# Kernel optimization log

Measured on AMD Instinct MI355X. Metric: run time of the kernel, lower is better.

The kernel has to match this reference:

```python
import jax, jax.numpy as jnp
from jax import lax
import numpy as np

NMS_THRESH = 0.5
SCORE_THRESH = 0.05
MAX_DET = 300
B, N, C, P = 8, 20000, 80, 51


def _iou_one_to_many(box, boxes):
    # box: (4,) in (x1,y1,x2,y2); boxes: (N,4). Same IoU math as tf.image.non_max_suppression.
    ix1 = jnp.maximum(box[0], boxes[:, 0])
    iy1 = jnp.maximum(box[1], boxes[:, 1])
    ix2 = jnp.minimum(box[2], boxes[:, 2])
    iy2 = jnp.minimum(box[3], boxes[:, 3])
    inter = jnp.maximum(ix2 - ix1, 0.0) * jnp.maximum(iy2 - iy1, 0.0)
    area_b = (box[2] - box[0]) * (box[3] - box[1])
    area_n = (boxes[:, 2] - boxes[:, 0]) * (boxes[:, 3] - boxes[:, 1])
    union = area_b + area_n - inter
    return jnp.where(union > 0.0, inter / union, 0.0)


def _greedy_nms(boxes, scores):
    """Fixed-length greedy NMS. scores already has -inf at entries below score threshold.
    Returns (idx, keep): idx (MAX_DET,) int32 selected box indices, keep (MAX_DET,) bool validity."""
    bx = lax.stop_gradient(boxes)           # NMS indices are non-differentiable
    s0 = lax.stop_gradient(scores)

    def step(s, _):
        i = jnp.argmax(s)
        ok = s[i] > -jnp.inf
        ious = _iou_one_to_many(bx[i], bx)
        s = jnp.where(ious > NMS_THRESH, -jnp.inf, s)
        s = s.at[i].set(-jnp.inf)
        return s, (i.astype(jnp.int32), ok)

    _, (idx, keep) = lax.scan(step, s0, None, length=MAX_DET)
    return idx, keep


def _filter_one(boxes, classification, relationship):
    # boxes (N,4), classification (N,C), relationship (N,P)
    n_cls = classification.shape[1]
    masked = jnp.where(classification > SCORE_THRESH, classification, -jnp.inf)  # (N,C)
    per_cls = masked.T                                                            # (C,N)

    # class-specific NMS, vectorized over classes
    idx, keep = jax.vmap(lambda s: _greedy_nms(boxes, s))(per_cls)  # (C,MAX_DET) each

    cand = jnp.take_along_axis(per_cls, idx.astype(jnp.int32), axis=1)  # (C,MAX_DET)
    cand = jnp.where(keep, cand, -jnp.inf)

    flat = cand.reshape(-1)                        # (C*MAX_DET,)
    top_s, top_pos = lax.top_k(flat, MAX_DET)      # global top-k over all classes
    box_idx = idx.reshape(-1)[top_pos]             # (MAX_DET,)
    label = top_pos // MAX_DET                     # class id (flatten order (C,M))
    valid = jnp.isfinite(top_s)

    out_boxes = jnp.where(valid[:, None], boxes[box_idx], -1.0)              # (MAX_DET,4)
    out_scores = jnp.where(valid, top_s, -1.0)                               # (MAX_DET,)
    out_labels = jnp.where(valid, label, -1).astype(jnp.int32)

    pred = relationship[box_idx]                                             # (MAX_DET,P)
    pred_labels = jnp.where(valid, jnp.argmax(pred, axis=1), -1).astype(jnp.int32)
    pred_scores = jnp.where(valid, jnp.max(pred, axis=1), -1.0)
    return out_boxes, out_scores, out_labels, pred_scores, pred_labels


def setup_inputs() -> dict:
    key = jax.random.key(0)
    k1, k2, k3, k4 = jax.random.split(key, 4)
    xy = jax.random.uniform(k1, (B, N, 2), dtype=jnp.float32) * 700.0
    wh = jax.random.uniform(k2, (B, N, 2), dtype=jnp.float32) * 100.0 + 1.0
    boxes = jnp.concatenate([xy, xy + wh], axis=-1)                   # valid (x1,y1,x2,y2)
    classification = jax.random.uniform(k3, (B, N, C), dtype=jnp.float32)
    relationship = jax.random.uniform(k4, (B, N, P), dtype=jnp.float32)
    return {"boxes": boxes, "classification": classification, "relationship": relationship}


def reference(boxes, classification, relationship):
    return jax.vmap(_filter_one)(boxes, classification, relationship)
```

## Files before the change

kernel.cpp:

```cpp
#include <hip/hip_runtime.h>
#include <hip/hip_bf16.h>
#include <math.h>

#define NBATCH 8
#define NBOX   20000
#define NCLS   80
#define NREL   51
#define MAXDET 300
#define NTOT   (NCLS * MAXDET)
#define CAP    512
#define SPECCAP 2560
#define NHB    3328
#define HB0    (0x3F666666u >> 9)
#define TARGETK 480u
#define SCORE_THR 0.05f
#define SPEC_THRF 0.9f
#define WWAVES 8

typedef unsigned long long u64;
typedef unsigned int u32;

__device__ __forceinline__ bool iou_sup(float ax1, float ay1, float ax2, float ay2, float aarea,
                                        float bx1, float by1, float bx2, float by2, float barea) {
  float ix1 = fmaxf(ax1, bx1);
  float iy1 = fmaxf(ay1, by1);
  float ix2 = fminf(ax2, bx2);
  float iy2 = fminf(ay2, by2);
  float dw = fmaxf(__fsub_rn(ix2, ix1), 0.0f);
  float dh = fmaxf(__fsub_rn(iy2, iy1), 0.0f);
  float inter = __fmul_rn(dw, dh);
  float uni = __fsub_rn(__fadd_rn(aarea, barea), inter);
  if (!(uni > 0.0f)) return false;
  return __fdiv_rn(inter, uni) > 0.5f;
}

__device__ __forceinline__ bool iou_gt_half(float ax1, float ay1, float ax2, float ay2,
                                            float bx1, float by1, float bx2, float by2) {
  float aa = __fmul_rn(__fsub_rn(ax2, ax1), __fsub_rn(ay2, ay1));
  float ab = __fmul_rn(__fsub_rn(bx2, bx1), __fsub_rn(by2, by1));
  return iou_sup(ax1, ay1, ax2, ay2, aa, bx1, by1, bx2, by2, ab);
}

__device__ __forceinline__ bool iou_sup_fast(float ax1, float ay1, float ax2, float ay2,
                                             float aarea, float bx1, float by1, float bx2,
                                             float by2, float barea) {
  float ix1 = fmaxf(ax1, bx1);
  float iy1 = fmaxf(ay1, by1);
  float ix2 = fminf(ax2, bx2);
  float iy2 = fminf(ay2, by2);
  float dw = fmaxf(__fsub_rn(ix2, ix1), 0.0f);
  float dh = fmaxf(__fsub_rn(iy2, iy1), 0.0f);
  float inter = __fmul_rn(dw, dh);
  float uni = __fsub_rn(__fadd_rn(aarea, barea), inter);
  return (uni > 0.0f) && (inter > __fmul_rn(0.5f, uni));
}

#define CEXR(x, y, asc) { bool sw_ = (asc) ? ((x) > (y)) : ((x) < (y)); \
                          if (sw_) { u64 t_ = (x); (x) = (y); (y) = t_; } }

__device__ __forceinline__ void bitonic_sort(u64* keys, int SZ, int tid) {
  for (int k = 2; k <= SZ; k <<= 1) {
    for (int j = k >> 1; j >= 4; j >>= 1) {
      for (int v = tid; v < (SZ >> 1); v += 256) {
        int i = ((v & ~(j - 1)) << 1) | (v & (j - 1));
        int p = i | j;
        bool asc = ((i & k) == 0);
        u64 a = keys[i], b = keys[p];
        bool sw = asc ? (a > b) : (a < b);
        if (sw) { keys[i] = b; keys[p] = a; }
      }
      __syncthreads();
    }
    if (tid < (SZ >> 2)) {
      ulonglong2* k2 = (ulonglong2*)keys;
      ulonglong2 lo = k2[tid * 2], hi = k2[tid * 2 + 1];
      u64 a = lo.x, b = lo.y, c = hi.x, d = hi.y;
      int i0 = tid << 2;
      if (k == 2) {
        CEXR(a, b, true); CEXR(c, d, false);
      } else {
        bool asc = ((i0 & k) == 0);
        CEXR(a, c, asc); CEXR(b, d, asc);
        CEXR(a, b, asc); CEXR(c, d, asc);
      }
      lo.x = a; lo.y = b; hi.x = c; hi.y = d;
      k2[tid * 2] = lo; k2[tid * 2 + 1] = hi;
    }
    __syncthreads();
  }
}

template <int NB>
__device__ __forceinline__ void suffix_fast(const u32* hist, u32 cap, u32* wsum4, u32* sout) {
  const int tid = threadIdx.x, lane = tid & 63, w = tid >> 6;
  const int G = NB / 256;
  u32 v = 0;
  const int hb = tid * G;
#pragma unroll
  for (int t = 0; t < G; ++t) v += hist[hb + t];
  u32 s = v;
#pragma unroll
  for (int off = 1; off < 64; off <<= 1) {
    u32 t2 = __shfl_down(s, off);
    if (lane + off < 64) s += t2;
  }
  if (lane == 0) wsum4[w] = s;
  __syncthreads();
  u32 total = wsum4[0] + wsum4[1] + wsum4[2] + wsum4[3];
  u32 after = 0;
#pragma unroll
  for (int ww = 1; ww < 4; ++ww) if (ww > w) after += wsum4[ww];
  u32 inc = s + after;
  u32 exc = inc - v;
  if (tid == 0) {
    sout[3] = total;
    if (total == 0u) { sout[0] = 0u; sout[1] = 0u; sout[2] = 0u; }
  }
  u32 target = total < cap ? total : cap;
  if (total != 0u && inc >= target && exc < target) {
    u32 acc = exc;
    for (int u = hb + G - 1; u >= hb; --u) {
      acc += hist[u];
      if (acc >= target) { sout[0] = (u32)u; sout[1] = acc; sout[2] = acc - hist[u]; break; }
    }
  }
  __syncthreads();
}

__global__ __launch_bounds__(256) void k_tr(const float* __restrict__ cls,
                                            float* __restrict__ colS,
                                            u32* __restrict__ ghist,
                                            u32* __restrict__ gtail) {
  __shared__ float tile[NCLS * 65];
  const int tid = threadIdx.x;
  const int b = blockIdx.y;
  const int n0 = blockIdx.x * 64;
  if (blockIdx.x == 0) {
    for (int i = tid; i < NHB; i += 256) ghist[b * NHB + i] = 0u;
    if (tid == 0) gtail[b] = 0u;
  }
  const int rows = (NBOX - n0) < 64 ? (NBOX - n0) : 64;
  const float4* src4 = (const float4*)(cls + ((size_t)b * NBOX + n0) * NCLS);
  const int nq = rows * (NCLS / 4);
  for (int i = tid; i < nq; i += 256) {
    int rr = i / (NCLS / 4);
    int c4 = i - rr * (NCLS / 4);
    float4 v = src4[i];
    tile[(c4 * 4 + 0) * 65 + rr] = v.x;
    tile[(c4 * 4 + 1) * 65 + rr] = v.y;
    tile[(c4 * 4 + 2) * 65 + rr] = v.z;
    tile[(c4 * 4 + 3) * 65 + rr] = v.w;
  }
  __syncthreads();
  float4* dst4 = (float4*)colS;
  for (int i = tid; i < NCLS * 16; i += 256) {
    int c = i >> 4, nl = i & 15;
    if (nl * 4 < rows) {
      float4 v;
      v.x = tile[c * 65 + nl * 4 + 0];
      v.y = tile[c * 65 + nl * 4 + 1];
      v.z = tile[c * 65 + nl * 4 + 2];
      v.w = tile[c * 65 + nl * 4 + 3];
      dst4[(((size_t)b * NCLS + c) * NBOX + n0) / 4 + nl] = v;
    }
  }
}

__global__ __launch_bounds__(256) void k_zero(u32* __restrict__ ghist,
                                              u32* __restrict__ gtail) {
  const int b = blockIdx.x;
  const int tid = threadIdx.x;
  for (int i = tid; i < NHB; i += 256) ghist[b * NHB + i] = 0u;
  if (tid == 0) gtail[b] = 0u;
}

template <int STRIDE>
__device__ __forceinline__ float4 load4s(const float* col, int q) {
  if (STRIDE == 1) return ((const float4*)col)[q];
  float4 v;
  v.x = col[(size_t)(q * 4 + 0) * STRIDE];
  v.y = col[(size_t)(q * 4 + 1) * STRIDE];
  v.z = col[(size_t)(q * 4 + 2) * STRIDE];
  v.w = col[(size_t)(q * 4 + 3) * STRIDE];
  return v;
}

template <int STRIDE>
__global__ __launch_bounds__(256) void k_sel(const float* __restrict__ scores,
                                             u64* __restrict__ keysBase, size_t kstride,
                                             int* __restrict__ selCnt,
                                             int* __restrict__ totCnt,
                                             int* __restrict__ flags) {
  __shared__ __align__(16) char smem[SPECCAP * 8 + NHB * 4 + CAP * 8];
  u64* side = (u64*)smem;
  u32* hist = (u32*)(smem + SPECCAP * 8);
  u64* keys = (u64*)(smem + SPECCAP * 8 + NHB * 4);
  __shared__ u32 wsum[4], selB[4], twave[4];
  __shared__ u32 s_scnt, s_cnt;

  const int tid = threadIdx.x;
  const int lane = tid & 63;
  const int w = tid >> 6;
  const u64 lmask = (1ull << lane) - 1ull;
  const int bc = blockIdx.x;
  const int b = bc / NCLS, c = bc % NCLS;
  const float* col = (STRIDE == 1) ? (scores + (size_t)bc * NBOX)
                                   : (scores + (size_t)b * NBOX * NCLS + c);

  for (int i = tid; i < NHB; i += 256) hist[i] = 0u;
  if (tid == 0) { s_scnt = 0u; s_cnt = 0u; }
  __syncthreads();

  u32 tailc = 0;
  for (int base = 0; base < NBOX / 4; base += 2048) {
    float4 v[8];
#pragma unroll
    for (int p = 0; p < 8; ++p) {
      int q = base + tid + (p << 8);
      if (q < NBOX / 4) v[p] = load4s<STRIDE>(col, q);
    }
#pragma unroll
    for (int p = 0; p < 8; ++p) {
      int q = base + tid + (p << 8);
      if (q < NBOX / 4) {
        float vv[4] = {v[p].x, v[p].y, v[p].z, v[p].w};
#pragma unroll
        for (int e = 0; e < 4; ++e) {
          float s = vv[e];
          bool spec = s > SPEC_THRF;
          if (s > SCORE_THR && !spec) ++tailc;
          u64 mb = __ballot(spec);
          if (mb) {
            u32 bs;
            if (lane == 0) bs = atomicAdd(&s_scnt, (u32)__popcll(mb));
            bs = __shfl(bs, 0);
            if (spec) {
              u32 bits = __float_as_uint(s);
              u32 pos = bs + (u32)__popcll(mb & lmask);
              if (pos < SPECCAP) side[pos] = ((u64)bits << 32) | (~(u32)(q * 4 + e));
              u32 h = (bits >> 9) - HB0;
              if (h > NHB - 1) h = NHB - 1;
              atomicAdd(&hist[h], 1u);
            }
          }
        }
      }
    }
  }
  u32 tr = tailc;
#pragma unroll
  for (int off = 1; off < 64; off <<= 1) tr += __shfl_down(tr, off);
  if (lane == 0) twave[w] = tr;
  __syncthreads();

  const u32 specCount = s_scnt;
  const u32 tailSum = twave[0] + twave[1] + twave[2] + twave[3];
  const u32 totalAll = specCount + tailSum;

  if (totalAll == 0u) {
    if (tid == 0) { selCnt[bc] = 0; totCnt[bc] = 0; flags[bc] = 0; }
    return;
  }
  const u32 target = totalAll < TARGETK ? totalAll : TARGETK;
  if (specCount < target || specCount > SPECCAP) {
    if (tid == 0) { selCnt[bc] = 0; totCnt[bc] = (int)totalAll; flags[bc] = 1; }
    return;
  }

  suffix_fast<NHB>(hist, target, wsum, selB);
  const u32 F0 = selB[0];
  const u32 selCount = selB[1];
  if (selCount > CAP) {
    if (tid == 0) { selCnt[bc] = 0; totCnt[bc] = (int)totalAll; flags[bc] = 1; }
    return;
  }

  const int iters = (int)((specCount + 255u) >> 8);
  for (int it2 = 0; it2 < iters; ++it2) {
    u32 idx = (u32)it2 * 256u + (u32)tid;
    bool act = idx < specCount;
    u64 key = act ? side[idx] : 0ull;
    u32 bits = (u32)(key >> 32);
    u32 h = (bits >> 9) - HB0;
    if (h > NHB - 1) h = NHB - 1;
    bool sel = act && (h >= F0);
    u64 ms = __ballot(sel);
    if (ms) {
      u32 bs;
      if (lane == 0) bs = atomicAdd(&s_cnt, (u32)__popcll(ms));
      bs = __shfl(bs, 0);
      if (sel) keys[bs + (u32)__popcll(ms & lmask)] = key;
    }
  }
  __syncthreads();
  for (int i = (int)selCount + tid; i < CAP; i += 256) keys[i] = 0ull;
  __syncthreads();

  bitonic_sort(keys, CAP, tid);

  u64* kout = keysBase + (size_t)bc * kstride;
  for (int i = tid; i < CAP; i += 256) kout[i] = keys[i];
  if (tid == 0) { selCnt[bc] = (int)selCount; totCnt[bc] = (int)totalAll; flags[bc] = 0; }
}

__device__ void slow_path(const float* __restrict__ boxes,
                          const float* __restrict__ cls, int bc,
                          float* __restrict__ keptScore, int* __restrict__ keptN,
                          int* __restrict__ keptCount,
                          u32* __restrict__ ghist, u32* __restrict__ gtail,
                          char* smem) {
  u32* sup = (u32*)smem;
  u64* red = (u64*)(smem + 2560);
  float4* sbx = (float4*)(smem + 6656);
  int* s_kept = (int*)(smem + 6672);
  const int tid = threadIdx.x;
  const int b = bc / NCLS, c = bc % NCLS;
  const float* col = cls + (size_t)b * NBOX * NCLS + c;

  for (int i = tid; i < (NBOX + 31) / 32; i += 512) sup[i] = 0u;
  if (tid == 0) *s_kept = 0;
  __syncthreads();
  for (int it = 0; it < MAXDET; ++it) {
    u64 best = 0ull;
    for (int n = tid; n < NBOX; n += 512) {
      if ((sup[n >> 5] >> (n & 31)) & 1u) continue;
      float s = col[(size_t)n * NCLS];
      if (s > SCORE_THR) {
        u64 key = ((u64)__float_as_uint(s) << 32) | (~(u32)n);
        if (key > best) best = key;
      }
    }
    red[tid] = best;
    __syncthreads();
    for (int off = 256; off > 0; off >>= 1) {
      if (tid < off) { u64 o = red[tid + off]; if (o > red[tid]) red[tid] = o; }
      __syncthreads();
    }
    u64 win = red[0];
    if (win == 0ull) break;
    u32 nw = ~((u32)win);
    if (tid == 0) {
      int k = *s_kept;
      keptScore[bc * MAXDET + k] = __uint_as_float((u32)(win >> 32));
      keptN[bc * MAXDET + k] = (int)nw;
      *s_kept = k + 1;
      *sbx = ((const float4*)boxes)[(size_t)b * NBOX + nw];
    }
    __syncthreads();
    float4 bx = *sbx;
    for (int n = tid; n < NBOX; n += 512) {
      float4 cb = ((const float4*)boxes)[(size_t)b * NBOX + n];
      if (iou_gt_half(bx.x, bx.y, bx.z, bx.w, cb.x, cb.y, cb.z, cb.w))
        atomicOr(&sup[n >> 5], 1u << (n & 31));
    }
    if (tid == 0) atomicOr(&sup[nw >> 5], 1u << (nw & 31));
    __syncthreads();
  }
  __syncthreads();
  const int kept = *s_kept;
  for (int r = kept + tid; r < MAXDET; r += 512) {
    keptScore[bc * MAXDET + r] = -INFINITY;
    keptN[bc * MAXDET + r] = 0;
  }
  for (int rr = tid; rr < kept; rr += 512) {
    float s = keptScore[bc * MAXDET + rr];
    if (s > SPEC_THRF) {
      u32 h = (__float_as_uint(s) >> 9) - HB0;
      if (h > NHB - 1) h = NHB - 1;
      atomicAdd(&ghist[b * NHB + h], 1u);
    } else {
      atomicAdd(&gtail[b], 1u);
    }
  }
  if (tid == 0) keptCount[bc] = kept;
}

__global__ __launch_bounds__(512) void k_walk(const float* __restrict__ boxes,
                                              const float* __restrict__ cls,
                                              const u64* __restrict__ keysBase, size_t kstride,
                                              const int* __restrict__ selCnt,
                                              const int* __restrict__ totCnt,
                                              float* __restrict__ keptScore,
                                              int* __restrict__ keptN,
                                              int* __restrict__ keptCount,
                                              const int* __restrict__ flags,
                                              u32* __restrict__ ghist,
                                              u32* __restrict__ gtail) {
  __shared__ __align__(16) char smem[22784];
  u64* keys = (u64*)smem;
  float4* candbox = (float4*)(smem + 4096);
  float* carea = (float*)(smem + 12288);
  float4* keptbox = (float4*)(smem + 14336);
  float* karea = (float*)(smem + 19136);
  int* kn = (int*)(smem + 20336);
  float* ksc = (float*)(smem + 21536);
  __shared__ u64 supW[WWAVES];
  __shared__ u64 mpart[WWAVES][64];
  __shared__ int s_kept;

  const int tid = threadIdx.x;
  const int lane = tid & 63;
  const int w = tid >> 6;
  const u64 lmask = (1ull << lane) - 1ull;
  const int bc = blockIdx.x;
  const int b = bc / NCLS;

  if (flags[bc] != 0) {
    slow_path(boxes, cls, bc, keptScore, keptN, keptCount, ghist, gtail, smem);
    return;
  }
  const u32 selCount = (u32)selCnt[bc];
  const u32 totalAll = (u32)totCnt[bc];

  const u64* kin = keysBase + (size_t)bc * kstride;
  for (int i = tid; i < CAP; i += 512) keys[i] = kin[i];
  if (tid == 0) s_kept = 0;
  __syncthreads();

  for (int i = tid; i < (int)selCount; i += 512) {
    int pos = CAP - 1 - i;
    u32 n = ~((u32)keys[pos]);
    float4 bb = ((const float4*)boxes)[(size_t)b * NBOX + n];
    candbox[pos] = bb;
    carea[pos] = __fmul_rn(__fsub_rn(bb.z, bb.x), __fsub_rn(bb.w, bb.y));
  }
  __syncthreads();

  const u32 ntile = (selCount + 63u) >> 6;
  for (u32 t = 0; t < ntile; ++t) {
    const int kept0 = s_kept;
    if (kept0 >= MAXDET) break;
    const u32 r = t * 64u + (u32)lane;
    const bool valid = r < selCount;
    const int si = valid ? (CAP - 1 - (int)r) : (CAP - 1);
    float4 mybox = candbox[si];
    float marea = carea[si];
    bool sup = false;
    for (int k = w; k < kept0; k += WWAVES) {
      float4 kb = keptbox[k];
      if (iou_sup_fast(kb.x, kb.y, kb.z, kb.w, karea[k],
                       mybox.x, mybox.y, mybox.z, mybox.w, marea))
        sup = true;
    }
    u64 bal = __ballot(sup);
    if (lane == 0) supW[w] = bal;
    u64 mw = 0ull;
    const int ebase = w * 8;
#pragma unroll
    for (int ee = 0; ee < 8; ++ee) {
      const int e = ebase + ee;
      int ei = CAP - 1 - (int)(t * 64u) - e;
      float4 eb = candbox[ei];
      if (e < lane && iou_sup_fast(eb.x, eb.y, eb.z, eb.w, carea[ei],
                                   mybox.x, mybox.y, mybox.z, mybox.w, marea))
        mw |= 1ull << e;
    }
    mpart[w][lane] = mw;
    __syncthreads();
    if (w == 0) {
      u64 prior = 0ull, m = 0ull;
#pragma unroll
      for (int ww = 0; ww < WWAVES; ++ww) {
        prior |= supW[ww];
        m |= mpart[ww][lane];
      }
      u64 remaining = __ballot(valid) & ~prior;
      u64 keptmask = 0ull;
      const int room = MAXDET - kept0;
      while (remaining != 0ull && (int)__popcll(keptmask) < room) {
        int j = __ffsll((long long)remaining) - 1;
        keptmask |= 1ull << j;
        remaining &= ~(1ull << j);
        u64 supj = __ballot(((m >> j) & 1ull) != 0ull);
        remaining &= ~supj;
      }
      if ((keptmask >> lane) & 1ull) {
        int pos = kept0 + (int)__popcll(keptmask & lmask);
        u64 mykey = keys[CAP - 1 - (int)r];
        keptbox[pos] = mybox;
        karea[pos] = marea;
        kn[pos] = (int)(~((u32)mykey));
        ksc[pos] = __uint_as_float((u32)(mykey >> 32));
      }
      if (lane == 0) s_kept = kept0 + (int)__popcll(keptmask);
    }
    __syncthreads();
  }

  const int kept = s_kept;
  const bool exhausted = (kept < MAXDET && selCount < totalAll);
  if (exhausted) {
    __syncthreads();
    slow_path(boxes, cls, bc, keptScore, keptN, keptCount, ghist, gtail, smem);
    return;
  }
  for (int rr = tid; rr < MAXDET; rr += 512) {
    keptScore[bc * MAXDET + rr] = (rr < kept) ? ksc[rr] : -INFINITY;
    keptN[bc * MAXDET + rr] = (rr < kept) ? kn[rr] : 0;
  }
  if (tid == 0) keptCount[bc] = kept;
  for (int rr = tid; rr < kept; rr += 512) {
    float s = ksc[rr];
    if (s > SPEC_THRF) {
      u32 h = (__float_as_uint(s) >> 9) - HB0;
      if (h > NHB - 1) h = NHB - 1;
      atomicAdd(&ghist[b * NHB + h], 1u);
    } else {
      atomicAdd(&gtail[b], 1u);
    }
  }
}

__global__ __launch_bounds__(256) void k_osort(const float* __restrict__ boxes,
                                               const float* __restrict__ rel,
                                               const float* __restrict__ keptScore,
                                               const int* __restrict__ keptN,
                                               const u32* __restrict__ ghist,
                                               const u32* __restrict__ gtail,
                                               float* __restrict__ out) {
  __shared__ u64 keys[1024];
  __shared__ u32 wsum[4], selB[4];
  __shared__ u32 s_cnt;
  const int tid = threadIdx.x;
  const int lane = tid & 63;
  const u64 lmask = (1ull << lane) - 1ull;
  const int b = blockIdx.x;
  const float4* ks4 = (const float4*)(keptScore + (size_t)b * NTOT);

  if (tid == 0) s_cnt = 0u;
  suffix_fast<NHB>(ghist + (size_t)b * NHB, (u32)MAXDET, wsum, selB);
  const u32 specTotal = selB[3];
  const u32 totalAll = specTotal + gtail[b];
  const u32 target = totalAll < (u32)MAXDET ? totalAll : (u32)MAXDET;
  const u32 F0 = selB[0];
  const u32 selSpec = selB[1];
  const bool fast = (totalAll != 0u) && (specTotal >= target) && (selSpec <= (u32)CAP);
  int SZ = CAP;

  if (totalAll != 0u) {
    if (fast) {
      for (int base = 0; base < NTOT / 4; base += 2048) {
        float4 v[8];
#pragma unroll
        for (int p = 0; p < 8; ++p) {
          int q = base + tid + (p << 8);
          if (q < NTOT / 4) v[p] = ks4[q];
        }
#pragma unroll
        for (int p = 0; p < 8; ++p) {
          int q = base + tid + (p << 8);
          if (q < NTOT / 4) {
            float vv[4] = {v[p].x, v[p].y, v[p].z, v[p].w};
#pragma unroll
            for (int e = 0; e < 4; ++e) {
              float s = vv[e];
              bool sel = false;
              u32 bits = 0;
              if (s > SPEC_THRF) {
                bits = __float_as_uint(s);
                u32 h = (bits >> 9) - HB0;
                if (h > NHB - 1) h = NHB - 1;
                sel = (h >= F0);
              }
              u64 ms = __ballot(sel);
              if (ms) {
                u32 bs;
                if (lane == 0) bs = atomicAdd(&s_cnt, (u32)__popcll(ms));
                bs = __shfl(bs, 0);
                if (sel)
                  keys[bs + (u32)__popcll(ms & lmask)] =
                      ((u64)bits << 32) | (~(u32)(q * 4 + e));
              }
            }
          }
        }
      }
      __syncthreads();
      for (int i = (int)selSpec + tid; i < CAP; i += 256) keys[i] = 0ull;
      __syncthreads();
      bitonic_sort(keys, CAP, tid);
      SZ = CAP;
    } else {
      if (tid < 64) {
        const int c0 = lane, c1 = 64 + lane;
        const bool has1 = (c1 < NCLS);
        const float* ls0 = keptScore + ((size_t)b * NCLS + c0) * MAXDET;
        const float* ls1 = keptScore + ((size_t)b * NCLS + (has1 ? c1 : c0)) * MAXDET;
        int h0 = 0, h1 = 0;
        float v0 = ls0[0], w0v = ls0[1];
        float v1 = has1 ? ls1[0] : -INFINITY;
        float w1v = has1 ? ls1[1] : -INFINITY;
        for (int r = 0; r < (int)target; ++r) {
          float bs; int bcl;
          if (has1 && v1 > v0) { bs = v1; bcl = c1; } else { bs = v0; bcl = c0; }
#pragma unroll
          for (int off = 32; off > 0; off >>= 1) {
            float os = __shfl_xor(bs, off);
            int oc = __shfl_xor(bcl, off);
            if (os > bs || (os == bs && oc < bcl)) { bs = os; bcl = oc; }
          }
          if (bcl == c0) {
            keys[1023 - r] = ((u64)__float_as_uint(bs) << 32) | (~(u32)(c0 * MAXDET + h0));
            ++h0; v0 = w0v; w0v = (h0 + 1 < MAXDET) ? ls0[h0 + 1] : -INFINITY;
          } else if (has1 && bcl == c1) {
            keys[1023 - r] = ((u64)__float_as_uint(bs) << 32) | (~(u32)(c1 * MAXDET + h1));
            ++h1; v1 = w1v; w1v = (h1 + 1 < MAXDET) ? ls1[h1 + 1] : -INFINITY;
          }
        }
      }
      __syncthreads();
      SZ = 1024;
    }
  }

  for (int r = tid; r < MAXDET; r += 256) {
    const bool valid = (u32)r < target;
    float s = -1.0f, pm = -1.0f, pl = -1.0f, cl = -1.0f;
    float4 ob; ob.x = ob.y = ob.z = ob.w = -1.0f;
    if (valid) {
      u64 key = keys[SZ - 1 - r];
      u32 fp = ~((u32)key);
      int c = (int)(fp / MAXDET);
      int slot = (int)(fp - (u32)c * MAXDET);
      int n = keptN[((size_t)b * NCLS + c) * MAXDET + slot];
      s = __uint_as_float((u32)(key >> 32));
      cl = (float)c;
      size_t nb = (size_t)b * NBOX + (u32)n;
      ob = ((const float4*)boxes)[nb];
      const float* rp = rel + nb * NREL;
      float vr[NREL];
#pragma unroll
      for (int p = 0; p < NREL; ++p) vr[p] = rp[p];
      float best = vr[0]; int bi = 0;
#pragma unroll
      for (int p = 1; p < NREL; ++p) { if (vr[p] > best) { best = vr[p]; bi = p; } }
      pm = best; pl = (float)bi;
    }
    ((float4*)out)[(size_t)b * MAXDET + r] = ob;
    const int sbase = NBATCH * MAXDET * 4;
    out[sbase + b * MAXDET + r] = s;
    out[sbase + NBATCH * MAXDET + b * MAXDET + r] = cl;
    out[sbase + 2 * NBATCH * MAXDET + b * MAXDET + r] = pm;
    out[sbase + 3 * NBATCH * MAXDET + b * MAXDET + r] = pl;
  }
}

extern "C" void kernel_launch(void* const* d_in, const int* in_sizes, int n_in,
                              void* d_out, int out_size, void* d_ws, size_t ws_size,
                              hipStream_t stream) {
  (void)in_sizes; (void)n_in; (void)out_size;
  const float* boxes = (const float*)d_in[0];
  const float* cls   = (const float*)d_in[1];
  const float* rel   = (const float*)d_in[2];
  float* out = (float*)d_out;
  char* ws = (char*)d_ws;

  const size_t trBytes = (size_t)NBATCH * NCLS * NBOX * 4;
  const size_t NP = NBATCH * NCLS;

  float* colS = (float*)ws;
  size_t off = 0;
  const size_t oKeptScore = off; off += NP * MAXDET * 4;
  const size_t oKeptN     = off; off += NP * MAXDET * 4;
  const size_t oKeptCount = off; off += NP * 4;
  const size_t oFlags     = off; off += NP * 4;
  const size_t oSelCnt    = off; off += NP * 4;
  const size_t oTotCnt    = off; off += NP * 4;
  const size_t oKeysSep   = off; off += NP * CAP * 8;
  const size_t oGhist     = off; off += (size_t)NBATCH * NHB * 4;
  const size_t oGtail     = off; off += NBATCH * 4;
  const size_t kbaseBytes = off;

  const bool useTr = ws_size >= trBytes + kbaseBytes;
  char* kbase = useTr ? (ws + trBytes) : ws;

  float* keptScore = (float*)(kbase + oKeptScore);
  int* keptN = (int*)(kbase + oKeptN);
  int* keptCount = (int*)(kbase + oKeptCount);
  int* flags = (int*)(kbase + oFlags);
  int* selCnt = (int*)(kbase + oSelCnt);
  int* totCnt = (int*)(kbase + oTotCnt);
  u64* keysSep = (u64*)(kbase + oKeysSep);
  u32* ghist = (u32*)(kbase + oGhist);
  u32* gtail = (u32*)(kbase + oGtail);

  u64* keysBase = useTr ? (u64*)colS : keysSep;
  const size_t kstride = useTr ? (size_t)(NBOX / 2) : (size_t)CAP;

  if (useTr) {
    k_tr<<<dim3((NBOX + 63) / 64, NBATCH), 256, 0, stream>>>(cls, colS, ghist, gtail);
    k_sel<1><<<NP, 256, 0, stream>>>(colS, keysBase, kstride, selCnt, totCnt, flags);
  } else {
    k_zero<<<NBATCH, 256, 0, stream>>>(ghist, gtail);
    k_sel<NCLS><<<NP, 256, 0, stream>>>(cls, keysBase, kstride, selCnt, totCnt, flags);
  }
  k_walk<<<NP, 512, 0, stream>>>(boxes, cls, keysBase, kstride, selCnt, totCnt,
                                 keptScore, keptN, keptCount, flags, ghist, gtail);
  k_osort<<<NBATCH, 256, 0, stream>>>(boxes, rel, keptScore, keptN, ghist, gtail, out);
}
```

Before: 140.3 us.

## Replace transpose+per-class select with row-major scatter into per-class buckets

Removes the full transpose of the classification tensor and the per-(batch,class) selection kernel. A new scatter kernel reads the classification rows coalesced, counts scores above threshold per class and appends high-score (>0.9) keys into global per-class buckets through global atomics. The histogram, threshold selection and bitonic sort move into the NMS kernel, which now runs them with 512 threads. This cuts one full read/write pass over the scores, at the cost of heavy global atomic contention on 640 counters and non-deterministic key order before sorting.

```diff
diff --git a/kernel.cpp b/kernel.cpp
--- a/kernel.cpp
+++ b/kernel.cpp
@@ -10,12 +10,14 @@
 #define NTOT   (NCLS * MAXDET)
 #define CAP    512
 #define SPECCAP 2560
-#define NHB    3328
+#define NHB    3584
 #define HB0    (0x3F666666u >> 9)
 #define TARGETK 480u
 #define SCORE_THR 0.05f
 #define SPEC_THRF 0.9f
 #define WWAVES 8
+#define QPB    5120
+#define QTOT   (NBOX * NCLS / 4)
 
 typedef unsigned long long u64;
 typedef unsigned int u32;
@@ -58,10 +60,11 @@
 #define CEXR(x, y, asc) { bool sw_ = (asc) ? ((x) > (y)) : ((x) < (y)); \
                           if (sw_) { u64 t_ = (x); (x) = (y); (y) = t_; } }
 
+template <int THREADS>
 __device__ __forceinline__ void bitonic_sort(u64* keys, int SZ, int tid) {
   for (int k = 2; k <= SZ; k <<= 1) {
     for (int j = k >> 1; j >= 4; j >>= 1) {
-      for (int v = tid; v < (SZ >> 1); v += 256) {
+      for (int v = tid; v < (SZ >> 1); v += THREADS) {
         int i = ((v & ~(j - 1)) << 1) | (v & (j - 1));
         int p = i | j;
         bool asc = ((i & k) == 0);
@@ -90,10 +93,11 @@
   }
 }
 
-template <int NB>
-__device__ __forceinline__ void suffix_fast(const u32* hist, u32 cap, u32* wsum4, u32* sout) {
+template <int NB, int THREADS>
+__device__ __forceinline__ void suffix_fast(const u32* hist, u32 cap, u32* wsum, u32* sout) {
   const int tid = threadIdx.x, lane = tid & 63, w = tid >> 6;
-  const int G = NB / 256;
+  const int NW = THREADS / 64;
+  const int G = NB / THREADS;
   u32 v = 0;
   const int hb = tid * G;
 #pragma unroll
@@ -104,12 +108,14 @@
     u32 t2 = __shfl_down(s, off);
     if (lane + off < 64) s += t2;
   }
-  if (lane == 0) wsum4[w] = s;
-  __syncthreads();
-  u32 total = wsum4[0] + wsum4[1] + wsum4[2] + wsum4[3];
+  if (lane == 0) wsum[w] = s;
+  __syncthreads();
+  u32 total = 0;
+#pragma unroll
+  for (int ww = 0; ww < NW; ++ww) total += wsum[ww];
   u32 after = 0;
 #pragma unroll
-  for (int ww = 1; ww < 4; ++ww) if (ww > w) after += wsum4[ww];
+  for (int ww = 1; ww < NW; ++ww) if (ww > w) after += wsum[ww];
   u32 inc = s + after;
   u32 exc = inc - v;
   if (tid == 0) {
@@ -127,180 +133,69 @@
   __syncthreads();
 }
 
-__global__ __launch_bounds__(256) void k_tr(const float* __restrict__ cls,
-                                            float* __restrict__ colS,
-                                            u32* __restrict__ ghist,
-                                            u32* __restrict__ gtail) {
-  __shared__ float tile[NCLS * 65];
-  const int tid = threadIdx.x;
-  const int b = blockIdx.y;
-  const int n0 = blockIdx.x * 64;
-  if (blockIdx.x == 0) {
-    for (int i = tid; i < NHB; i += 256) ghist[b * NHB + i] = 0u;
-    if (tid == 0) gtail[b] = 0u;
-  }
-  const int rows = (NBOX - n0) < 64 ? (NBOX - n0) : 64;
-  const float4* src4 = (const float4*)(cls + ((size_t)b * NBOX + n0) * NCLS);
-  const int nq = rows * (NCLS / 4);
-  for (int i = tid; i < nq; i += 256) {
-    int rr = i / (NCLS / 4);
-    int c4 = i - rr * (NCLS / 4);
-    float4 v = src4[i];
-    tile[(c4 * 4 + 0) * 65 + rr] = v.x;
-    tile[(c4 * 4 + 1) * 65 + rr] = v.y;
-    tile[(c4 * 4 + 2) * 65 + rr] = v.z;
-    tile[(c4 * 4 + 3) * 65 + rr] = v.w;
-  }
-  __syncthreads();
-  float4* dst4 = (float4*)colS;
-  for (int i = tid; i < NCLS * 16; i += 256) {
-    int c = i >> 4, nl = i & 15;
-    if (nl * 4 < rows) {
-      float4 v;
-      v.x = tile[c * 65 + nl * 4 + 0];
-      v.y = tile[c * 65 + nl * 4 + 1];
-      v.z = tile[c * 65 + nl * 4 + 2];
-      v.w = tile[c * 65 + nl * 4 + 3];
-      dst4[(((size_t)b * NCLS + c) * NBOX + n0) / 4 + nl] = v;
-    }
-  }
-}
-
-__global__ __launch_bounds__(256) void k_zero(u32* __restrict__ ghist,
-                                              u32* __restrict__ gtail) {
+__global__ __launch_bounds__(256) void k_init(u32* __restrict__ ghist,
+                                              u32* __restrict__ gtail,
+                                              u32* __restrict__ bucketCnt,
+                                              u32* __restrict__ totCnt) {
   const int b = blockIdx.x;
   const int tid = threadIdx.x;
   for (int i = tid; i < NHB; i += 256) ghist[b * NHB + i] = 0u;
   if (tid == 0) gtail[b] = 0u;
-}
-
-template <int STRIDE>
-__device__ __forceinline__ float4 load4s(const float* col, int q) {
-  if (STRIDE == 1) return ((const float4*)col)[q];
-  float4 v;
-  v.x = col[(size_t)(q * 4 + 0) * STRIDE];
-  v.y = col[(size_t)(q * 4 + 1) * STRIDE];
-  v.z = col[(size_t)(q * 4 + 2) * STRIDE];
-  v.w = col[(size_t)(q * 4 + 3) * STRIDE];
-  return v;
-}
-
-template <int STRIDE>
-__global__ __launch_bounds__(256) void k_sel(const float* __restrict__ scores,
-                                             u64* __restrict__ keysBase, size_t kstride,
-                                             int* __restrict__ selCnt,
-                                             int* __restrict__ totCnt,
-                                             int* __restrict__ flags) {
-  __shared__ __align__(16) char smem[SPECCAP * 8 + NHB * 4 + CAP * 8];
-  u64* side = (u64*)smem;
-  u32* hist = (u32*)(smem + SPECCAP * 8);
-  u64* keys = (u64*)(smem + SPECCAP * 8 + NHB * 4);
-  __shared__ u32 wsum[4], selB[4], twave[4];
-  __shared__ u32 s_scnt, s_cnt;
-
+  for (int i = tid; i < NCLS; i += 256) {
+    bucketCnt[b * NCLS + i] = 0u;
+    totCnt[b * NCLS + i] = 0u;
+  }
+}
+
+__global__ __launch_bounds__(256) void k_scatter(const float* __restrict__ cls,
+                                                 u64* __restrict__ bucketKeys,
+                                                 u32* __restrict__ bucketCnt,
+                                                 u32* __restrict__ totCnt) {
+  __shared__ u32 cnt80[NCLS];
   const int tid = threadIdx.x;
-  const int lane = tid & 63;
-  const int w = tid >> 6;
-  const u64 lmask = (1ull << lane) - 1ull;
-  const int bc = blockIdx.x;
-  const int b = bc / NCLS, c = bc % NCLS;
-  const float* col = (STRIDE == 1) ? (scores + (size_t)bc * NBOX)
-                                   : (scores + (size_t)b * NBOX * NCLS + c);
-
-  for (int i = tid; i < NHB; i += 256) hist[i] = 0u;
-  if (tid == 0) { s_scnt = 0u; s_cnt = 0u; }
-  __syncthreads();
-
-  u32 tailc = 0;
-  for (int base = 0; base < NBOX / 4; base += 2048) {
+  const int b = blockIdx.y;
+  const int q0 = blockIdx.x * QPB;
+  const int qend = (q0 + QPB < QTOT) ? (q0 + QPB) : QTOT;
+  const float4* src = (const float4*)(cls + (size_t)b * NBOX * NCLS);
+  for (int i = tid; i < NCLS; i += 256) cnt80[i] = 0u;
+  __syncthreads();
+
+  for (int base = q0; base < qend; base += 2048) {
     float4 v[8];
 #pragma unroll
     for (int p = 0; p < 8; ++p) {
       int q = base + tid + (p << 8);
-      if (q < NBOX / 4) v[p] = load4s<STRIDE>(col, q);
+      if (q < qend) v[p] = src[q];
     }
 #pragma unroll
     for (int p = 0; p < 8; ++p) {
       int q = base + tid + (p << 8);
-      if (q < NBOX / 4) {
+      if (q < qend) {
+        int n = q / (NCLS / 4);
+        int cb = (q % (NCLS / 4)) * 4;
         float vv[4] = {v[p].x, v[p].y, v[p].z, v[p].w};
 #pragma unroll
         for (int e = 0; e < 4; ++e) {
           float s = vv[e];
-          bool spec = s > SPEC_THRF;
-          if (s > SCORE_THR && !spec) ++tailc;
-          u64 mb = __ballot(spec);
-          if (mb) {
-            u32 bs;
-            if (lane == 0) bs = atomicAdd(&s_scnt, (u32)__popcll(mb));
-            bs = __shfl(bs, 0);
-            if (spec) {
-              u32 bits = __float_as_uint(s);
-              u32 pos = bs + (u32)__popcll(mb & lmask);
-              if (pos < SPECCAP) side[pos] = ((u64)bits << 32) | (~(u32)(q * 4 + e));
-              u32 h = (bits >> 9) - HB0;
-              if (h > NHB - 1) h = NHB - 1;
-              atomicAdd(&hist[h], 1u);
+          if (s > SCORE_THR) {
+            atomicAdd(&cnt80[cb + e], 1u);
+            if (s > SPEC_THRF) {
+              int bkt = b * NCLS + cb + e;
+              u32 pos = atomicAdd(&bucketCnt[bkt], 1u);
+              if (pos < SPECCAP)
+                bucketKeys[(size_t)bkt * SPECCAP + pos] =
+                    ((u64)__float_as_uint(s) << 32) | (~(u32)n);
             }
           }
         }
       }
     }
   }
-  u32 tr = tailc;
-#pragma unroll
-  for (int off = 1; off < 64; off <<= 1) tr += __shfl_down(tr, off);
-  if (lane == 0) twave[w] = tr;
-  __syncthreads();
-
-  const u32 specCount = s_scnt;
-  const u32 tailSum = twave[0] + twave[1] + twave[2] + twave[3];
-  const u32 totalAll = specCount + tailSum;
-
-  if (totalAll == 0u) {
-    if (tid == 0) { selCnt[bc] = 0; totCnt[bc] = 0; flags[bc] = 0; }
-    return;
-  }
-  const u32 target = totalAll < TARGETK ? totalAll : TARGETK;
-  if (specCount < target || specCount > SPECCAP) {
-    if (tid == 0) { selCnt[bc] = 0; totCnt[bc] = (int)totalAll; flags[bc] = 1; }
-    return;
-  }
-
-  suffix_fast<NHB>(hist, target, wsum, selB);
-  const u32 F0 = selB[0];
-  const u32 selCount = selB[1];
-  if (selCount > CAP) {
-    if (tid == 0) { selCnt[bc] = 0; totCnt[bc] = (int)totalAll; flags[bc] = 1; }
-    return;
-  }
-
-  const int iters = (int)((specCount + 255u) >> 8);
-  for (int it2 = 0; it2 < iters; ++it2) {
-    u32 idx = (u32)it2 * 256u + (u32)tid;
-    bool act = idx < specCount;
-    u64 key = act ? side[idx] : 0ull;
-    u32 bits = (u32)(key >> 32);
-    u32 h = (bits >> 9) - HB0;
-    if (h > NHB - 1) h = NHB - 1;
-    bool sel = act && (h >= F0);
-    u64 ms = __ballot(sel);
-    if (ms) {
-      u32 bs;
-      if (lane == 0) bs = atomicAdd(&s_cnt, (u32)__popcll(ms));
-      bs = __shfl(bs, 0);
-      if (sel) keys[bs + (u32)__popcll(ms & lmask)] = key;
-    }
-  }
-  __syncthreads();
-  for (int i = (int)selCount + tid; i < CAP; i += 256) keys[i] = 0ull;
-  __syncthreads();
-
-  bitonic_sort(keys, CAP, tid);
-
-  u64* kout = keysBase + (size_t)bc * kstride;
-  for (int i = tid; i < CAP; i += 256) kout[i] = keys[i];
-  if (tid == 0) { selCnt[bc] = (int)selCount; totCnt[bc] = (int)totalAll; flags[bc] = 0; }
+  __syncthreads();
+  for (int c = tid; c < NCLS; c += 256) {
+    u32 v = cnt80[c];
+    if (v) atomicAdd(&totCnt[b * NCLS + c], v);
+  }
 }
 
 __device__ void slow_path(const float* __restrict__ boxes,
@@ -375,25 +270,28 @@
   if (tid == 0) keptCount[bc] = kept;
 }
 
-__global__ __launch_bounds__(512) void k_walk(const float* __restrict__ boxes,
-                                              const float* __restrict__ cls,
-                                              const u64* __restrict__ keysBase, size_t kstride,
-                                              const int* __restrict__ selCnt,
-                                              const int* __restrict__ totCnt,
-                                              float* __restrict__ keptScore,
-                                              int* __restrict__ keptN,
-                                              int* __restrict__ keptCount,
-                                              const int* __restrict__ flags,
-                                              u32* __restrict__ ghist,
-                                              u32* __restrict__ gtail) {
-  __shared__ __align__(16) char smem[22784];
-  u64* keys = (u64*)smem;
-  float4* candbox = (float4*)(smem + 4096);
-  float* carea = (float*)(smem + 12288);
-  float4* keptbox = (float4*)(smem + 14336);
-  float* karea = (float*)(smem + 19136);
-  int* kn = (int*)(smem + 20336);
-  float* ksc = (float*)(smem + 21536);
+__global__ __launch_bounds__(512) void k_nms(const float* __restrict__ boxes,
+                                             const float* __restrict__ cls,
+                                             const u64* __restrict__ bucketKeys,
+                                             const u32* __restrict__ bucketCnt,
+                                             const u32* __restrict__ totCnt,
+                                             float* __restrict__ keptScore,
+                                             int* __restrict__ keptN,
+                                             int* __restrict__ keptCount,
+                                             u32* __restrict__ ghist,
+                                             u32* __restrict__ gtail) {
+  __shared__ __align__(16) char smem[38912];
+  u64* side = (u64*)smem;
+  u32* hist = (u32*)(smem + 20480);
+  u64* keys = (u64*)(smem + 34816);
+  float4* candbox = (float4*)smem;
+  float* carea = (float*)(smem + 8192);
+  float4* keptbox = (float4*)(smem + 10240);
+  float* karea = (float*)(smem + 15040);
+  int* kn = (int*)(smem + 16240);
+  float* ksc = (float*)(smem + 17440);
+  __shared__ u32 wsum[WWAVES], selB[4];
+  __shared__ u32 s_cnt;
   __shared__ u64 supW[WWAVES];
   __shared__ u64 mpart[WWAVES][64];
   __shared__ int s_kept;
@@ -405,17 +303,68 @@
   const int bc = blockIdx.x;
   const int b = bc / NCLS;
 
-  if (flags[bc] != 0) {
+  const u32 specRaw = bucketCnt[bc];
+  const u32 totalAll = totCnt[bc];
+
+  if (totalAll == 0u) {
+    for (int r = tid; r < MAXDET; r += 512) {
+      keptScore[bc * MAXDET + r] = -INFINITY;
+      keptN[bc * MAXDET + r] = 0;
+    }
+    if (tid == 0) keptCount[bc] = 0;
+    return;
+  }
+  const u32 target = totalAll < TARGETK ? totalAll : TARGETK;
+  if (specRaw > SPECCAP || specRaw < target) {
     slow_path(boxes, cls, bc, keptScore, keptN, keptCount, ghist, gtail, smem);
     return;
   }
-  const u32 selCount = (u32)selCnt[bc];
-  const u32 totalAll = (u32)totCnt[bc];
-
-  const u64* kin = keysBase + (size_t)bc * kstride;
-  for (int i = tid; i < CAP; i += 512) keys[i] = kin[i];
-  if (tid == 0) s_kept = 0;
-  __syncthreads();
+  const u32 specCount = specRaw;
+
+  const u64* bk = bucketKeys + (size_t)bc * SPECCAP;
+  for (int i = tid; i < (int)specCount; i += 512) side[i] = bk[i];
+  for (int i = tid; i < NHB; i += 512) hist[i] = 0u;
+  if (tid == 0) { s_cnt = 0u; s_kept = 0; }
+  __syncthreads();
+  for (int i = tid; i < (int)specCount; i += 512) {
+    u32 bits = (u32)(side[i] >> 32);
+    u32 h = (bits >> 9) - HB0;
+    if (h > NHB - 1) h = NHB - 1;
+    atomicAdd(&hist[h], 1u);
+  }
+  __syncthreads();
+
+  suffix_fast<NHB, 512>(hist, target, wsum, selB);
+  const u32 F0 = selB[0];
+  const u32 selCount = selB[1];
+  if (selCount > CAP) {
+    __syncthreads();
+    slow_path(boxes, cls, bc, keptScore, keptN, keptCount, ghist, gtail, smem);
+    return;
+  }
+
+  const int iters = (int)((specCount + 511u) >> 9);
+  for (int it2 = 0; it2 < iters; ++it2) {
+    u32 idx = (u32)it2 * 512u + (u32)tid;
+    bool act = idx < specCount;
+    u64 key = act ? side[idx] : 0ull;
+    u32 bits = (u32)(key >> 32);
+    u32 h = (bits >> 9) - HB0;
+    if (h > NHB - 1) h = NHB - 1;
+    bool sel = act && (h >= F0);
+    u64 ms = __ballot(sel);
+    if (ms) {
+      u32 bs;
+      if (lane == 0) bs = atomicAdd(&s_cnt, (u32)__popcll(ms));
+      bs = __shfl(bs, 0);
+      if (sel) keys[bs + (u32)__popcll(ms & lmask)] = key;
+    }
+  }
+  __syncthreads();
+  for (int i = (int)selCount + tid; i < CAP; i += 512) keys[i] = 0ull;
+  __syncthreads();
+
+  bitonic_sort<512>(keys, CAP, tid);
 
   for (int i = tid; i < (int)selCount; i += 512) {
     int pos = CAP - 1 - i;
@@ -528,7 +477,7 @@
   const float4* ks4 = (const float4*)(keptScore + (size_t)b * NTOT);
 
   if (tid == 0) s_cnt = 0u;
-  suffix_fast<NHB>(ghist + (size_t)b * NHB, (u32)MAXDET, wsum, selB);
+  suffix_fast<NHB, 256>(ghist + (size_t)b * NHB, (u32)MAXDET, wsum, selB);
   const u32 specTotal = selB[3];
   const u32 totalAll = specTotal + gtail[b];
   const u32 target = totalAll < (u32)MAXDET ? totalAll : (u32)MAXDET;
@@ -578,7 +527,7 @@
       __syncthreads();
       for (int i = (int)selSpec + tid; i < CAP; i += 256) keys[i] = 0ull;
       __syncthreads();
-      bitonic_sort(keys, CAP, tid);
+      bitonic_sort<256>(keys, CAP, tid);
       SZ = CAP;
     } else {
       if (tid < 64) {
@@ -648,53 +597,40 @@
 extern "C" void kernel_launch(void* const* d_in, const int* in_sizes, int n_in,
                               void* d_out, int out_size, void* d_ws, size_t ws_size,
                               hipStream_t stream) {
-  (void)in_sizes; (void)n_in; (void)out_size;
+  (void)in_sizes; (void)n_in; (void)out_size; (void)ws_size;
   const float* boxes = (const float*)d_in[0];
   const float* cls   = (const float*)d_in[1];
   const float* rel   = (const float*)d_in[2];
   float* out = (float*)d_out;
   char* ws = (char*)d_ws;
 
-  const size_t trBytes = (size_t)NBATCH * NCLS * NBOX * 4;
   const size_t NP = NBATCH * NCLS;
-
-  float* colS = (float*)ws;
   size_t off = 0;
   const size_t oKeptScore = off; off += NP * MAXDET * 4;
   const size_t oKeptN     = off; off += NP * MAXDET * 4;
   const size_t oKeptCount = off; off += NP * 4;
-  const size_t oFlags     = off; off += NP * 4;
-  const size_t oSelCnt    = off; off += NP * 4;
+  const size_t oBucketCnt = off; off += NP * 4;
   const size_t oTotCnt    = off; off += NP * 4;
-  const size_t oKeysSep   = off; off += NP * CAP * 8;
+  const size_t oGtail     = off; off += NBATCH * 4;
+  off = (off + 7) & ~(size_t)7;
   const size_t oGhist     = off; off += (size_t)NBATCH * NHB * 4;
-  const size_t oGtail     = off; off += NBATCH * 4;
-  const size_t kbaseBytes = off;
-
-  const bool useTr = ws_size >= trBytes + kbaseBytes;
-  char* kbase = useTr ? (ws + trBytes) : ws;
-
-  float* keptScore = (float*)(kbase + oKeptScore);
-  int* keptN = (int*)(kbase + oKeptN);
-  int* keptCount = (int*)(kbase + oKeptCount);
-  int* flags = (int*)(kbase + oFlags);
-  int* selCnt = (int*)(kbase + oSelCnt);
-  int* totCnt = (int*)(kbase + oTotCnt);
-  u64* keysSep = (u64*)(kbase + oKeysSep);
-  u32* ghist = (u32*)(kbase + oGhist);
-  u32* gtail = (u32*)(kbase + oGtail);
-
-  u64* keysBase = useTr ? (u64*)colS : keysSep;
-  const size_t kstride = useTr ? (size_t)(NBOX / 2) : (size_t)CAP;
-
-  if (useTr) {
-    k_tr<<<dim3((NBOX + 63) / 64, NBATCH), 256, 0, stream>>>(cls, colS, ghist, gtail);
-    k_sel<1><<<NP, 256, 0, stream>>>(colS, keysBase, kstride, selCnt, totCnt, flags);
-  } else {
-    k_zero<<<NBATCH, 256, 0, stream>>>(ghist, gtail);
-    k_sel<NCLS><<<NP, 256, 0, stream>>>(cls, keysBase, kstride, selCnt, totCnt, flags);
-  }
-  k_walk<<<NP, 512, 0, stream>>>(boxes, cls, keysBase, kstride, selCnt, totCnt,
-                                 keptScore, keptN, keptCount, flags, ghist, gtail);
+  off = (off + 7) & ~(size_t)7;
+  const size_t oBucketKeys = off; off += NP * SPECCAP * 8;
+
+  float* keptScore = (float*)(ws + oKeptScore);
+  int* keptN = (int*)(ws + oKeptN);
+  int* keptCount = (int*)(ws + oKeptCount);
+  u32* bucketCnt = (u32*)(ws + oBucketCnt);
+  u32* totCnt = (u32*)(ws + oTotCnt);
+  u32* gtail = (u32*)(ws + oGtail);
+  u32* ghist = (u32*)(ws + oGhist);
+  u64* bucketKeys = (u64*)(ws + oBucketKeys);
+
+  const int qBlocks = (QTOT + QPB - 1) / QPB;
+
+  k_init<<<NBATCH, 256, 0, stream>>>(ghist, gtail, bucketCnt, totCnt);
+  k_scatter<<<dim3(qBlocks, NBATCH), 256, 0, stream>>>(cls, bucketKeys, bucketCnt, totCnt);
+  k_nms<<<NP, 512, 0, stream>>>(boxes, cls, bucketKeys, bucketCnt, totCnt,
+                                keptScore, keptN, keptCount, ghist, gtail);
   k_osort<<<NBATCH, 256, 0, stream>>>(boxes, rel, keptScore, keptN, ghist, gtail, out);
 }
```

Measured after the change: 526.8 us. 3.76x slower.
